# Kernel optimization log

Measured on AMD Instinct MI355X. Metric: run time of the kernel, lower is better.

## Reference

```python
import jax, jax.numpy as jnp
import numpy as np

NUM_HEADS = 32
NUM_KV_HEADS = 8  # num_heads // 4 (GQA)
HEAD_DIM = 64     # hidden_size // num_heads
ROPE_BASE = 10000.0


def _rotate_half(x):
    x1, x2 = jnp.split(x, 2, axis=-1)
    return jnp.concatenate((-x2, x1), axis=-1)


def _rope_cos_sin(seq_len, dtype):
    inv_freq = 1.0 / (ROPE_BASE ** (jnp.arange(0, HEAD_DIM, 2, dtype=jnp.float32) / HEAD_DIM))
    t = jnp.arange(seq_len, dtype=jnp.float32)
    freqs = jnp.outer(t, inv_freq)                 # [S, HEAD_DIM//2]
    emb = jnp.concatenate((freqs, freqs), axis=-1) # [S, HEAD_DIM]
    return jnp.cos(emb).astype(dtype), jnp.sin(emb).astype(dtype)


def setup_inputs() -> dict:
    key = jax.random.key(0)
    ks = jax.random.split(key, 5)
    B, S, H = 1, 2048, 2048
    KV = NUM_KV_HEADS * HEAD_DIM  # 512
    s = 0.02
    return {
        "hidden_states": jax.random.normal(ks[0], (B, S, H), jnp.float32),
        "Wq": jax.random.normal(ks[1], (H, H), jnp.float32) * s,
        "Wk": jax.random.normal(ks[2], (KV, H), jnp.float32) * s,
        "Wv": jax.random.normal(ks[3], (KV, H), jnp.float32) * s,
        "Wo": jax.random.normal(ks[4], (H, H), jnp.float32) * s,
    }


def reference(hidden_states, Wq, Wk, Wv, Wo):
    B, S, H = hidden_states.shape
    dtype = hidden_states.dtype
    # QKV projections (nn.Linear with weight [out,in], no bias)
    q = jnp.einsum("bsh,oh->bso", hidden_states, Wq)
    k = jnp.einsum("bsh,oh->bso", hidden_states, Wk)
    v = jnp.einsum("bsh,oh->bso", hidden_states, Wv)
    q = q.reshape(B, S, NUM_HEADS, HEAD_DIM).transpose(0, 2, 1, 3)      # [B,H,S,D]
    k = k.reshape(B, S, NUM_KV_HEADS, HEAD_DIM).transpose(0, 2, 1, 3)   # [B,KV,S,D]
    v = v.reshape(B, S, NUM_KV_HEADS, HEAD_DIM).transpose(0, 2, 1, 3)
    # RoPE
    cos, sin = _rope_cos_sin(S, dtype)  # [S,D] broadcast over batch/heads
    q = q * cos + _rotate_half(q) * sin
    k = k * cos + _rotate_half(k) * sin
    # GQA: repeat_interleave KV heads
    groups = NUM_HEADS // NUM_KV_HEADS
    k = jnp.repeat(k, groups, axis=1)
    v = jnp.repeat(v, groups, axis=1)
    # Attention: scores in fp32 softmax, causal mask (additive)
    scale = 1.0 / np.sqrt(HEAD_DIM)
    scores = jnp.einsum("bhqd,bhkd->bhqk", q, k) * scale
    causal = jnp.tril(jnp.ones((S, S), dtype=bool))
    scores = jnp.where(causal, scores, jnp.finfo(jnp.float32).min)
    probs = jax.nn.softmax(scores.astype(jnp.float32), axis=-1).astype(dtype)
    attn = jnp.einsum("bhqk,bhkd->bhqd", probs, v)
    attn = attn.transpose(0, 2, 1, 3).reshape(B, S, H)
    return jnp.einsum("bsh,oh->bso", attn, Wo)
```

## Files before the change

### kernel.cpp

```cpp
#include <hip/hip_runtime.h>
#include <hip/hip_bf16.h>
#include <math.h>

typedef __hip_bfloat16 bf16;
typedef __attribute__((ext_vector_type(8))) short short8;
typedef __attribute__((ext_vector_type(4))) short short4v;
typedef __attribute__((ext_vector_type(4))) float floatx4;

#define MFMA16(a, b, c) __builtin_amdgcn_mfma_f32_16x16x32_bf16((a), (b), (c), 0, 0, 0)

typedef const __attribute__((address_space(1))) void* as1_cvp;
typedef __attribute__((address_space(3))) void* as3_vp;

__device__ __forceinline__ void gload_lds16(const bf16* g, bf16* lds_uni) {
    __builtin_amdgcn_global_load_lds((as1_cvp)g, (as3_vp)lds_uni, 16, 0, 0);
}

__global__ __launch_bounds__(256) void cvt_all(
    const float* __restrict__ a0, const float* __restrict__ a1,
    const float* __restrict__ a2, const float* __restrict__ a3,
    const float* __restrict__ a4,
    bf16* __restrict__ d0, bf16* __restrict__ d1, bf16* __restrict__ d2,
    bf16* __restrict__ d3, bf16* __restrict__ d4)
{
    const int b = blockIdx.x;
    const float* src; bf16* dst; int off;
    if (b < 2048)      { src = a0; dst = d0; off = b; }
    else if (b < 4096) { src = a1; dst = d1; off = b - 2048; }
    else if (b < 4608) { src = a2; dst = d2; off = b - 4096; }
    else if (b < 5120) { src = a3; dst = d3; off = b - 4608; }
    else               { src = a4; dst = d4; off = b - 5120; }
    const int i = (off * 256 + threadIdx.x) * 8;
    const float4 x = *(const float4*)(src + i);
    const float4 y = *(const float4*)(src + i + 4);
    bf16 t[8];
    t[0] = __float2bfloat16(x.x); t[1] = __float2bfloat16(x.y);
    t[2] = __float2bfloat16(x.z); t[3] = __float2bfloat16(x.w);
    t[4] = __float2bfloat16(y.x); t[5] = __float2bfloat16(y.y);
    t[6] = __float2bfloat16(y.z); t[7] = __float2bfloat16(y.w);
    *(short8*)(dst + i) = *(const short8*)t;
}

#define GEMM_STAGE6(k0, sA, sB)                                                 \
    gload_lds16(gA + (k0),            (sA));                                    \
    gload_lds16(gA + A64 + (k0),      (sA) + 2048);                             \
    gload_lds16(gB + (k0),            (sB));                                    \
    gload_lds16(gA + (k0) + 32,       (sA) + 4096);                             \
    gload_lds16(gA + A64 + (k0) + 32, (sA) + 6144);                             \
    gload_lds16(gB + (k0) + 32,       (sB) + 2048);

#define GEMM_K_LOOP_DB(KB)                                                      \
    {                                                                           \
        bf16* sA0 = &As[0][0] + w * 512; bf16* sB0 = &Bs[0][0] + w * 512;       \
        bf16* sA1 = &As[1][0] + w * 512; bf16* sB1 = &Bs[1][0] + w * 512;       \
        GEMM_STAGE6(0, sA0, sB0)                                                \
        for (int k0 = 0; k0 < (KB); k0 += 64) {                                 \
            const int cur = (k0 >> 6) & 1;                                      \
            if (k0 + 64 < (KB)) {                                               \
                if (cur == 0) { GEMM_STAGE6(k0 + 64, sA1, sB1) }                \
                else          { GEMM_STAGE6(k0 + 64, sA0, sB0) }                \
                asm volatile("s_waitcnt vmcnt(6)" ::: "memory");                \
            } else {                                                            \
                asm volatile("s_waitcnt vmcnt(0)" ::: "memory");                \
            }                                                                   \
            __builtin_amdgcn_s_barrier();                                       \
            const bf16* Acur = &As[cur][0];                                     \
            const bf16* Bcur = &Bs[cur][0];                                     \
            _Pragma("unroll")                                                   \
            for (int hh = 0; hh < 2; ++hh) {                                    \
                short8 af[2], bfr[4];                                           \
                _Pragma("unroll")                                               \
                for (int i = 0; i < 2; ++i)                                     \
                    af[i] = *(const short8*)&Acur[hh * 4096 + (w * 32 + i * 16 + l15) * 32 + quad * 8]; \
                _Pragma("unroll")                                               \
                for (int j = 0; j < 4; ++j)                                     \
                    bfr[j] = *(const short8*)&Bcur[hh * 2048 + (j * 16 + l15) * 32 + quad * 8]; \
                _Pragma("unroll")                                               \
                for (int i = 0; i < 2; ++i)                                     \
                    _Pragma("unroll")                                           \
                    for (int j = 0; j < 4; ++j)                                 \
                        acc[i][j] = MFMA16(af[i], bfr[j], acc[i][j]);           \
            }                                                                   \
            __builtin_amdgcn_s_barrier();                                       \
        }                                                                       \
    }

__global__ __launch_bounds__(256) void gemm_qkv(
    const bf16* __restrict__ A, const bf16* __restrict__ Wq,
    const bf16* __restrict__ Wk, const bf16* __restrict__ Wv,
    bf16* __restrict__ qb, bf16* __restrict__ kb, bf16* __restrict__ vt)
{
    constexpr int LDK = 2048;
    __shared__ bf16 As[2][128 * 64];
    __shared__ bf16 Bs[2][64 * 64];

    const int tid  = threadIdx.x;
    const int lane = tid & 63;
    const int w    = tid >> 6;
    const int quad = lane >> 4, l15 = lane & 15;
    const int bx = blockIdx.x, by = blockIdx.y;

    const bf16* Bp; int bxl, mode;
    if (bx < 32)      { Bp = Wq; bxl = bx;      mode = 0; }
    else if (bx < 40) { Bp = Wk; bxl = bx - 32; mode = 1; }
    else              { Bp = Wv; bxl = bx - 40; mode = 2; }

    floatx4 acc[2][4];
#pragma unroll
    for (int i = 0; i < 2; ++i)
#pragma unroll
        for (int j = 0; j < 4; ++j) {
            floatx4 z = {0.f, 0.f, 0.f, 0.f};
            acc[i][j] = z;
        }

    const int srow = tid >> 2;
    const int sch  = (tid & 3) * 8;
    const bf16* gA = A  + (size_t)(by * 128 + srow) * LDK + sch;
    const bf16* gB = Bp + (size_t)(bxl * 64 + srow) * LDK + sch;
    const size_t A64 = (size_t)64 * LDK;

    GEMM_K_LOOP_DB(LDK)

    if (mode == 2) {
#pragma unroll
        for (int i = 0; i < 2; ++i)
#pragma unroll
            for (int j = 0; j < 4; ++j) {
                const int col = bxl * 64 + j * 16 + l15;
                const int rowb = by * 128 + w * 32 + i * 16 + quad * 4;
                bf16 t[4];
#pragma unroll
                for (int r = 0; r < 4; ++r) t[r] = __float2bfloat16(acc[i][j][r]);
                *(short4v*)&vt[(size_t)col * 2048 + rowb] = *(const short4v*)t;
            }
    } else {
        bf16* C = (mode == 0) ? qb : kb;
        const int Nn = (mode == 0) ? 2048 : 512;
        const float scale = (mode == 0) ? 0.125f : 1.0f;
        const float LOG2_1E4 = 13.28771237954945f;
        const float ifr0 = exp2f(-((float)l15) * (LOG2_1E4 / 32.f));
        const float ifr1 = exp2f(-((float)(16 + l15)) * (LOG2_1E4 / 32.f));
#pragma unroll
        for (int i = 0; i < 2; ++i) {
#pragma unroll
            for (int r = 0; r < 4; ++r) {
                const int row = by * 128 + w * 32 + i * 16 + quad * 4 + r;
                float s0, c0, s1, c1;
                sincosf((float)row * ifr0, &s0, &c0);
                sincosf((float)row * ifr1, &s1, &c1);
#pragma unroll
                for (int j = 0; j < 4; ++j) {
                    const float x  = acc[i][j][r];
                    const float xp = acc[i][j ^ 2][r];
                    const float cs = (j & 1) ? c1 : c0;
                    const float sn = (j & 1) ? s1 : s0;
                    const float oo = (x * cs + ((j < 2) ? -xp : xp) * sn) * scale;
                    const int col = bxl * 64 + j * 16 + l15;
                    C[(size_t)row * Nn + col] = __float2bfloat16(oo);
                }
            }
        }
    }
}

__global__ __launch_bounds__(256) void gemm_out(
    const bf16* __restrict__ A, const bf16* __restrict__ B, float* __restrict__ C)
{
    constexpr int LDK = 2048;
    __shared__ bf16 As[2][128 * 64];
    __shared__ bf16 Bs[2][64 * 64];

    const int tid  = threadIdx.x;
    const int lane = tid & 63;
    const int w    = tid >> 6;
    const int quad = lane >> 4, l15 = lane & 15;
    const int bx = blockIdx.x, by = blockIdx.y;

    floatx4 acc[2][4];
#pragma unroll
    for (int i = 0; i < 2; ++i)
#pragma unroll
        for (int j = 0; j < 4; ++j) {
            floatx4 z = {0.f, 0.f, 0.f, 0.f};
            acc[i][j] = z;
        }

    const int srow = tid >> 2;
    const int sch  = (tid & 3) * 8;
    const bf16* gA = A + (size_t)(by * 128 + srow) * LDK + sch;
    const bf16* gB = B + (size_t)(bx * 64 + srow) * LDK + sch;
    const size_t A64 = (size_t)64 * LDK;

    GEMM_K_LOOP_DB(LDK)

#pragma unroll
    for (int i = 0; i < 2; ++i)
#pragma unroll
        for (int j = 0; j < 4; ++j)
#pragma unroll
            for (int r = 0; r < 4; ++r) {
                const int row = by * 128 + w * 32 + i * 16 + quad * 4 + r;
                const int col = bx * 64 + j * 16 + l15;
                C[(size_t)row * 2048 + col] = acc[i][j][r];
            }
}

__global__ __launch_bounds__(256) void fattn9(
    const bf16* __restrict__ q, const bf16* __restrict__ k,
    const bf16* __restrict__ vt, bf16* __restrict__ o)
{
    __shared__ bf16 Ks[2][64 * 68];
    __shared__ bf16 Vs[2][64 * 68];
    __shared__ bf16 Ps[4][16 * 68];

    const int tpair = blockIdx.x;
    const int h = blockIdx.y;
    const int kvh = h >> 2;
    const int tid = threadIdx.x, lane = tid & 63, w = tid >> 6;
    const int quad = lane >> 4, l15 = lane & 15;
    bf16* P = Ps[w];

    short ob[8];
#pragma unroll
    for (int e = 0; e < 8; ++e) ob[e] = (short)0x3F80;
    const short8 ones = *(const short8*)ob;

    const int srow = tid >> 3;
    const int ch8  = (tid & 7) * 8;
    const bf16* kg = k  + (size_t)kvh * 64 + ch8;
    const bf16* vg = vt + (size_t)(kvh * 64 + srow) * 2048 + ch8;

#pragma unroll 1
    for (int ph = 0; ph < 2; ++ph) {
        const int a = ph ? (31 - tpair) : tpair;
        const int qrow0 = a * 64 + w * 16;

        short8 qf[2];
#pragma unroll
        for (int ks = 0; ks < 2; ++ks)
            qf[ks] = *(const short8*)&q[(size_t)(qrow0 + l15) * 2048 + h * 64 + ks * 32 + quad * 8];

        floatx4 o_acc[4], l_acc;
#pragma unroll
        for (int n4 = 0; n4 < 4; ++n4) {
            floatx4 z = {0.f, 0.f, 0.f, 0.f};
            o_acc[n4] = z;
        }
        { floatx4 z = {0.f, 0.f, 0.f, 0.f}; l_acc = z; }

        {
            short8 k0 = *(const short8*)(kg + (size_t)srow * 512);
            short8 k1 = *(const short8*)(kg + (size_t)(srow + 32) * 512);
            short8 v0 = *(const short8*)(vg);
            short8 v1 = *(const short8*)(vg + (size_t)32 * 2048);
            *(short8*)&Ks[0][srow * 68 + ch8]        = k0;
            *(short8*)&Ks[0][(srow + 32) * 68 + ch8] = k1;
            *(short8*)&Vs[0][srow * 68 + ch8]        = v0;
            *(short8*)&Vs[0][(srow + 32) * 68 + ch8] = v1;
        }
        __syncthreads();

        for (int kt = 0; kt <= a; ++kt) {
            const int buf = kt & 1;

            short8 nk0, nk1, nv0, nv1;
            if (kt < a) {
                const size_t kr = (size_t)((kt + 1) * 64) * 512;
                nk0 = *(const short8*)(kg + kr + (size_t)srow * 512);
                nk1 = *(const short8*)(kg + kr + (size_t)(srow + 32) * 512);
                nv0 = *(const short8*)(vg + (kt + 1) * 64);
                nv1 = *(const short8*)(vg + (size_t)32 * 2048 + (kt + 1) * 64);
            }

            floatx4 s_acc[4];
#pragma unroll
            for (int n = 0; n < 4; ++n) {
                floatx4 z = {0.f, 0.f, 0.f, 0.f};
                s_acc[n] = z;
            }
#pragma unroll
            for (int n = 0; n < 4; ++n)
#pragma unroll
                for (int ks = 0; ks < 2; ++ks) {
                    const short8 kf = *(const short8*)&Ks[buf][(n * 16 + l15) * 68 + ks * 32 + quad * 8];
                    s_acc[n] = MFMA16(kf, qf[ks], s_acc[n]);
                }

            if (kt < a) {
#pragma unroll
                for (int n = 0; n < 4; ++n) {
                    bf16 t4[4];
#pragma unroll
                    for (int r = 0; r < 4; ++r)
                        t4[r] = __float2bfloat16(__expf(s_acc[n][r]));
                    *(short4v*)&P[l15 * 68 + n * 16 + quad * 4] = *(const short4v*)t4;
                }
            } else {
#pragma unroll
                for (int n = 0; n < 4; ++n) {
                    bf16 t4[4];
#pragma unroll
                    for (int r = 0; r < 4; ++r) {
                        const bool okc = (n * 16 + quad * 4 + r) <= (w * 16 + l15);
                        t4[r] = __float2bfloat16(okc ? __expf(s_acc[n][r]) : 0.f);
                    }
                    *(short4v*)&P[l15 * 68 + n * 16 + quad * 4] = *(const short4v*)t4;
                }
            }

#pragma unroll
            for (int ks2 = 0; ks2 < 2; ++ks2) {
                const short8 pf = *(const short8*)&P[l15 * 68 + ks2 * 32 + quad * 8];
                l_acc = MFMA16(pf, ones, l_acc);
#pragma unroll
                for (int n4 = 0; n4 < 4; ++n4) {
                    const short8 vf = *(const short8*)&Vs[buf][(n4 * 16 + l15) * 68 + ks2 * 32 + quad * 8];
                    o_acc[n4] = MFMA16(pf, vf, o_acc[n4]);
                }
            }

            if (kt < a) {
                *(short8*)&Ks[buf ^ 1][srow * 68 + ch8]        = nk0;
                *(short8*)&Ks[buf ^ 1][(srow + 32) * 68 + ch8] = nk1;
                *(short8*)&Vs[buf ^ 1][srow * 68 + ch8]        = nv0;
                *(short8*)&Vs[buf ^ 1][(srow + 32) * 68 + ch8] = nv1;
            }
            __syncthreads();
        }

#pragma unroll
        for (int n4 = 0; n4 < 4; ++n4)
#pragma unroll
            for (int r = 0; r < 4; ++r) {
                const float val = o_acc[n4][r] / l_acc[r];
                const int row = qrow0 + quad * 4 + r;
                const int col = h * 64 + n4 * 16 + l15;
                o[(size_t)row * 2048 + col] = __float2bfloat16(val);
            }
    }
}

extern "C" void kernel_launch(void* const* d_in, const int* in_sizes, int n_in,
                              void* d_out, int out_size, void* d_ws, size_t ws_size,
                              hipStream_t stream)
{
    const float* hs = (const float*)d_in[0];
    const float* Wq = (const float*)d_in[1];
    const float* Wk = (const float*)d_in[2];
    const float* Wv = (const float*)d_in[3];
    const float* Wo = (const float*)d_in[4];
    float* out = (float*)d_out;

    bf16* ws  = (bf16*)d_ws;
    bf16* hsb = ws;
    bf16* Wqb = ws + 4194304;
    bf16* Wkb = ws + 8388608;
    bf16* Wvb = ws + 9437184;
    bf16* Wob = ws + 10485760;
    bf16* qb  = ws + 14680064;
    bf16* kb  = ws + 18874368;
    bf16* vtb = ws + 19922944;
    bf16* ab  = ws + 20971520;

    dim3 blk(256);
    cvt_all<<<7168, blk, 0, stream>>>(hs, Wq, Wk, Wv, Wo, hsb, Wqb, Wkb, Wvb, Wob);
    gemm_qkv<<<dim3(48, 16), blk, 0, stream>>>(hsb, Wqb, Wkb, Wvb, qb, kb, vtb);
    fattn9<<<dim3(16, 32), blk, 0, stream>>>(qb, kb, vtb, ab);
    gemm_out<<<dim3(32, 16), blk, 0, stream>>>(ab, Wob, out);
}
```

Before: 219.6 us.

## Split attention into 32-row query tiles with 128-thread blocks

The flash-attention kernel now gives each block a 32-row query tile with two waves instead of a 64-row tile with four, and doubles the grid to 32x32 blocks. Each block still pairs a short and a long causal tile to balance work, and the causal mask now compares absolute query and key positions. The aim is more blocks to fill the CUs and finer causal granularity. The cost is that each block loads a full 64-row K/V tile for only 32 query rows, which doubles K/V traffic per query.

```diff
diff --git a/kernel.cpp b/kernel.cpp
--- a/kernel.cpp
+++ b/kernel.cpp
@@ -206,15 +206,15 @@
             }
 }
 
-__global__ __launch_bounds__(256) void fattn9(
+__global__ __launch_bounds__(128) void fattn10(
     const bf16* __restrict__ q, const bf16* __restrict__ k,
     const bf16* __restrict__ vt, bf16* __restrict__ o)
 {
     __shared__ bf16 Ks[2][64 * 68];
     __shared__ bf16 Vs[2][64 * 68];
-    __shared__ bf16 Ps[4][16 * 68];
-
-    const int tpair = blockIdx.x;
+    __shared__ bf16 Ps[2][16 * 68];
+
+    const int tp = blockIdx.x;
     const int h = blockIdx.y;
     const int kvh = h >> 2;
     const int tid = threadIdx.x, lane = tid & 63, w = tid >> 6;
@@ -233,8 +233,9 @@
 
 #pragma unroll 1
     for (int ph = 0; ph < 2; ++ph) {
-        const int a = ph ? (31 - tpair) : tpair;
-        const int qrow0 = a * 64 + w * 16;
+        const int a = ph ? (63 - tp) : tp;
+        const int nkt = (a >> 1) + 1;
+        const int qrow0 = a * 32 + w * 16;
 
         short8 qf[2];
 #pragma unroll
@@ -250,27 +251,26 @@
         { floatx4 z = {0.f, 0.f, 0.f, 0.f}; l_acc = z; }
 
         {
-            short8 k0 = *(const short8*)(kg + (size_t)srow * 512);
-            short8 k1 = *(const short8*)(kg + (size_t)(srow + 32) * 512);
-            short8 v0 = *(const short8*)(vg);
-            short8 v1 = *(const short8*)(vg + (size_t)32 * 2048);
-            *(short8*)&Ks[0][srow * 68 + ch8]        = k0;
-            *(short8*)&Ks[0][(srow + 32) * 68 + ch8] = k1;
-            *(short8*)&Vs[0][srow * 68 + ch8]        = v0;
-            *(short8*)&Vs[0][(srow + 32) * 68 + ch8] = v1;
+#pragma unroll
+            for (int jj = 0; jj < 4; ++jj) {
+                short8 kv_ = *(const short8*)(kg + (size_t)(srow + 16 * jj) * 512);
+                short8 vv_ = *(const short8*)(vg + (size_t)(16 * jj) * 2048);
+                *(short8*)&Ks[0][(srow + 16 * jj) * 68 + ch8] = kv_;
+                *(short8*)&Vs[0][(srow + 16 * jj) * 68 + ch8] = vv_;
+            }
         }
         __syncthreads();
 
-        for (int kt = 0; kt <= a; ++kt) {
+        for (int kt = 0; kt < nkt; ++kt) {
             const int buf = kt & 1;
 
-            short8 nk0, nk1, nv0, nv1;
-            if (kt < a) {
-                const size_t kr = (size_t)((kt + 1) * 64) * 512;
-                nk0 = *(const short8*)(kg + kr + (size_t)srow * 512);
-                nk1 = *(const short8*)(kg + kr + (size_t)(srow + 32) * 512);
-                nv0 = *(const short8*)(vg + (kt + 1) * 64);
-                nv1 = *(const short8*)(vg + (size_t)32 * 2048 + (kt + 1) * 64);
+            short8 nk[4], nv[4];
+            if (kt + 1 < nkt) {
+#pragma unroll
+                for (int jj = 0; jj < 4; ++jj) {
+                    nk[jj] = *(const short8*)(kg + (size_t)((kt + 1) * 64 + srow + 16 * jj) * 512);
+                    nv[jj] = *(const short8*)(vg + (size_t)(16 * jj) * 2048 + (kt + 1) * 64);
+                }
             }
 
             floatx4 s_acc[4];
@@ -287,7 +287,7 @@
                     s_acc[n] = MFMA16(kf, qf[ks], s_acc[n]);
                 }
 
-            if (kt < a) {
+            if (kt + 1 < nkt) {
 #pragma unroll
                 for (int n = 0; n < 4; ++n) {
                     bf16 t4[4];
@@ -297,13 +297,14 @@
                     *(short4v*)&P[l15 * 68 + n * 16 + quad * 4] = *(const short4v*)t4;
                 }
             } else {
+                const int qg = qrow0 + l15;
 #pragma unroll
                 for (int n = 0; n < 4; ++n) {
                     bf16 t4[4];
 #pragma unroll
                     for (int r = 0; r < 4; ++r) {
-                        const bool okc = (n * 16 + quad * 4 + r) <= (w * 16 + l15);
-                        t4[r] = __float2bfloat16(okc ? __expf(s_acc[n][r]) : 0.f);
+                        const int sg = kt * 64 + n * 16 + quad * 4 + r;
+                        t4[r] = __float2bfloat16((sg <= qg) ? __expf(s_acc[n][r]) : 0.f);
                     }
                     *(short4v*)&P[l15 * 68 + n * 16 + quad * 4] = *(const short4v*)t4;
                 }
@@ -320,11 +321,12 @@
                 }
             }
 
-            if (kt < a) {
-                *(short8*)&Ks[buf ^ 1][srow * 68 + ch8]        = nk0;
-                *(short8*)&Ks[buf ^ 1][(srow + 32) * 68 + ch8] = nk1;
-                *(short8*)&Vs[buf ^ 1][srow * 68 + ch8]        = nv0;
-                *(short8*)&Vs[buf ^ 1][(srow + 32) * 68 + ch8] = nv1;
+            if (kt + 1 < nkt) {
+#pragma unroll
+                for (int jj = 0; jj < 4; ++jj) {
+                    *(short8*)&Ks[buf ^ 1][(srow + 16 * jj) * 68 + ch8] = nk[jj];
+                    *(short8*)&Vs[buf ^ 1][(srow + 16 * jj) * 68 + ch8] = nv[jj];
+                }
             }
             __syncthreads();
         }
@@ -366,6 +368,6 @@
     dim3 blk(256);
     cvt_all<<<7168, blk, 0, stream>>>(hs, Wq, Wk, Wv, Wo, hsb, Wqb, Wkb, Wvb, Wob);
     gemm_qkv<<<dim3(48, 16), blk, 0, stream>>>(hsb, Wqb, Wkb, Wvb, qb, kb, vtb);
-    fattn9<<<dim3(16, 32), blk, 0, stream>>>(qb, kb, vtb, ab);
+    fattn10<<<dim3(32, 32), dim3(128), 0, stream>>>(qb, kb, vtb, ab);
     gemm_out<<<dim3(32, 16), blk, 0, stream>>>(ab, Wob, out);
 }
```

New measurement: 225.8 us. 1.03x slower.

## Enlarge GEMM tiles to 128x128 with 2x2 wave layout and BK 32

Applied to the files above, without the earlier changes.

Both projection GEMMs switch from 128x64 output tiles with a K-step of 64 to 128x128 tiles with a K-step of 32. Each wave now computes a 64x64 sub-tile, and grids are halved accordingly. The aim is more operand reuse per LDS load and fewer global bytes per FLOP. The cost is fewer blocks, which leaves gemm_out at one block per CU, plus twice as many barriers per K.

```diff
diff --git a/kernel.cpp b/kernel.cpp
--- a/kernel.cpp
+++ b/kernel.cpp
@@ -41,73 +41,69 @@
     *(short8*)(dst + i) = *(const short8*)t;
 }
 
-#define GEMM_STAGE6(k0, sA, sB)                                                 \
-    gload_lds16(gA + (k0),            (sA));                                    \
-    gload_lds16(gA + A64 + (k0),      (sA) + 2048);                             \
-    gload_lds16(gB + (k0),            (sB));                                    \
-    gload_lds16(gA + (k0) + 32,       (sA) + 4096);                             \
-    gload_lds16(gA + A64 + (k0) + 32, (sA) + 6144);                             \
-    gload_lds16(gB + (k0) + 32,       (sB) + 2048);
-
-#define GEMM_K_LOOP_DB(KB)                                                      \
+#define GEMM_STAGE4(k0, sA, sB)                                                 \
+    gload_lds16(gA + (k0),       (sA));                                         \
+    gload_lds16(gA + K64 + (k0), (sA) + 2048);                                  \
+    gload_lds16(gB + (k0),       (sB));                                         \
+    gload_lds16(gB + K64 + (k0), (sB) + 2048);
+
+#define GEMM_K_LOOP_DB128(KB)                                                   \
     {                                                                           \
         bf16* sA0 = &As[0][0] + w * 512; bf16* sB0 = &Bs[0][0] + w * 512;       \
         bf16* sA1 = &As[1][0] + w * 512; bf16* sB1 = &Bs[1][0] + w * 512;       \
-        GEMM_STAGE6(0, sA0, sB0)                                                \
-        for (int k0 = 0; k0 < (KB); k0 += 64) {                                 \
-            const int cur = (k0 >> 6) & 1;                                      \
-            if (k0 + 64 < (KB)) {                                               \
-                if (cur == 0) { GEMM_STAGE6(k0 + 64, sA1, sB1) }                \
-                else          { GEMM_STAGE6(k0 + 64, sA0, sB0) }                \
-                asm volatile("s_waitcnt vmcnt(6)" ::: "memory");                \
+        GEMM_STAGE4(0, sA0, sB0)                                                \
+        for (int k0 = 0; k0 < (KB); k0 += 32) {                                 \
+            const int cur = (k0 >> 5) & 1;                                      \
+            if (k0 + 32 < (KB)) {                                               \
+                if (cur == 0) { GEMM_STAGE4(k0 + 32, sA1, sB1) }                \
+                else          { GEMM_STAGE4(k0 + 32, sA0, sB0) }                \
+                asm volatile("s_waitcnt vmcnt(4)" ::: "memory");                \
             } else {                                                            \
                 asm volatile("s_waitcnt vmcnt(0)" ::: "memory");                \
             }                                                                   \
             __builtin_amdgcn_s_barrier();                                       \
             const bf16* Acur = &As[cur][0];                                     \
             const bf16* Bcur = &Bs[cur][0];                                     \
+            short8 af[4], bfr[4];                                               \
             _Pragma("unroll")                                                   \
-            for (int hh = 0; hh < 2; ++hh) {                                    \
-                short8 af[2], bfr[4];                                           \
-                _Pragma("unroll")                                               \
-                for (int i = 0; i < 2; ++i)                                     \
-                    af[i] = *(const short8*)&Acur[hh * 4096 + (w * 32 + i * 16 + l15) * 32 + quad * 8]; \
+            for (int i = 0; i < 4; ++i)                                         \
+                af[i] = *(const short8*)&Acur[(wr * 64 + i * 16 + l15) * 32 + quad * 8]; \
+            _Pragma("unroll")                                                   \
+            for (int j = 0; j < 4; ++j)                                         \
+                bfr[j] = *(const short8*)&Bcur[(wc * 64 + j * 16 + l15) * 32 + quad * 8]; \
+            _Pragma("unroll")                                                   \
+            for (int i = 0; i < 4; ++i)                                         \
                 _Pragma("unroll")                                               \
                 for (int j = 0; j < 4; ++j)                                     \
-                    bfr[j] = *(const short8*)&Bcur[hh * 2048 + (j * 16 + l15) * 32 + quad * 8]; \
-                _Pragma("unroll")                                               \
-                for (int i = 0; i < 2; ++i)                                     \
-                    _Pragma("unroll")                                           \
-                    for (int j = 0; j < 4; ++j)                                 \
-                        acc[i][j] = MFMA16(af[i], bfr[j], acc[i][j]);           \
-            }                                                                   \
+                    acc[i][j] = MFMA16(af[i], bfr[j], acc[i][j]);               \
             __builtin_amdgcn_s_barrier();                                       \
         }                                                                       \
     }
 
-__global__ __launch_bounds__(256) void gemm_qkv(
+__global__ __launch_bounds__(256, 4) void gemm_qkv(
     const bf16* __restrict__ A, const bf16* __restrict__ Wq,
     const bf16* __restrict__ Wk, const bf16* __restrict__ Wv,
     bf16* __restrict__ qb, bf16* __restrict__ kb, bf16* __restrict__ vt)
 {
     constexpr int LDK = 2048;
-    __shared__ bf16 As[2][128 * 64];
-    __shared__ bf16 Bs[2][64 * 64];
+    __shared__ bf16 As[2][128 * 32];
+    __shared__ bf16 Bs[2][128 * 32];
 
     const int tid  = threadIdx.x;
     const int lane = tid & 63;
     const int w    = tid >> 6;
+    const int wr   = w >> 1, wc = w & 1;
     const int quad = lane >> 4, l15 = lane & 15;
     const int bx = blockIdx.x, by = blockIdx.y;
 
     const bf16* Bp; int bxl, mode;
-    if (bx < 32)      { Bp = Wq; bxl = bx;      mode = 0; }
-    else if (bx < 40) { Bp = Wk; bxl = bx - 32; mode = 1; }
-    else              { Bp = Wv; bxl = bx - 40; mode = 2; }
-
-    floatx4 acc[2][4];
-#pragma unroll
-    for (int i = 0; i < 2; ++i)
+    if (bx < 16)      { Bp = Wq; bxl = bx;      mode = 0; }
+    else if (bx < 20) { Bp = Wk; bxl = bx - 16; mode = 1; }
+    else              { Bp = Wv; bxl = bx - 20; mode = 2; }
+
+    floatx4 acc[4][4];
+#pragma unroll
+    for (int i = 0; i < 4; ++i)
 #pragma unroll
         for (int j = 0; j < 4; ++j) {
             floatx4 z = {0.f, 0.f, 0.f, 0.f};
@@ -117,18 +113,18 @@
     const int srow = tid >> 2;
     const int sch  = (tid & 3) * 8;
     const bf16* gA = A  + (size_t)(by * 128 + srow) * LDK + sch;
-    const bf16* gB = Bp + (size_t)(bxl * 64 + srow) * LDK + sch;
-    const size_t A64 = (size_t)64 * LDK;
-
-    GEMM_K_LOOP_DB(LDK)
+    const bf16* gB = Bp + (size_t)(bxl * 128 + srow) * LDK + sch;
+    const size_t K64 = (size_t)64 * LDK;
+
+    GEMM_K_LOOP_DB128(LDK)
 
     if (mode == 2) {
 #pragma unroll
-        for (int i = 0; i < 2; ++i)
+        for (int i = 0; i < 4; ++i)
 #pragma unroll
             for (int j = 0; j < 4; ++j) {
-                const int col = bxl * 64 + j * 16 + l15;
-                const int rowb = by * 128 + w * 32 + i * 16 + quad * 4;
+                const int col = bxl * 128 + wc * 64 + j * 16 + l15;
+                const int rowb = by * 128 + wr * 64 + i * 16 + quad * 4;
                 bf16 t[4];
 #pragma unroll
                 for (int r = 0; r < 4; ++r) t[r] = __float2bfloat16(acc[i][j][r]);
@@ -142,10 +138,10 @@
         const float ifr0 = exp2f(-((float)l15) * (LOG2_1E4 / 32.f));
         const float ifr1 = exp2f(-((float)(16 + l15)) * (LOG2_1E4 / 32.f));
 #pragma unroll
-        for (int i = 0; i < 2; ++i) {
+        for (int i = 0; i < 4; ++i) {
 #pragma unroll
             for (int r = 0; r < 4; ++r) {
-                const int row = by * 128 + w * 32 + i * 16 + quad * 4 + r;
+                const int row = by * 128 + wr * 64 + i * 16 + quad * 4 + r;
                 float s0, c0, s1, c1;
                 sincosf((float)row * ifr0, &s0, &c0);
                 sincosf((float)row * ifr1, &s1, &c1);
@@ -156,7 +152,7 @@
                     const float cs = (j & 1) ? c1 : c0;
                     const float sn = (j & 1) ? s1 : s0;
                     const float oo = (x * cs + ((j < 2) ? -xp : xp) * sn) * scale;
-                    const int col = bxl * 64 + j * 16 + l15;
+                    const int col = bxl * 128 + wc * 64 + j * 16 + l15;
                     C[(size_t)row * Nn + col] = __float2bfloat16(oo);
                 }
             }
@@ -164,22 +160,23 @@
     }
 }
 
-__global__ __launch_bounds__(256) void gemm_out(
+__global__ __launch_bounds__(256, 4) void gemm_out(
     const bf16* __restrict__ A, const bf16* __restrict__ B, float* __restrict__ C)
 {
     constexpr int LDK = 2048;
-    __shared__ bf16 As[2][128 * 64];
-    __shared__ bf16 Bs[2][64 * 64];
+    __shared__ bf16 As[2][128 * 32];
+    __shared__ bf16 Bs[2][128 * 32];
 
     const int tid  = threadIdx.x;
     const int lane = tid & 63;
     const int w    = tid >> 6;
+    const int wr   = w >> 1, wc = w & 1;
     const int quad = lane >> 4, l15 = lane & 15;
     const int bx = blockIdx.x, by = blockIdx.y;
 
-    floatx4 acc[2][4];
-#pragma unroll
-    for (int i = 0; i < 2; ++i)
+    floatx4 acc[4][4];
+#pragma unroll
+    for (int i = 0; i < 4; ++i)
 #pragma unroll
         for (int j = 0; j < 4; ++j) {
             floatx4 z = {0.f, 0.f, 0.f, 0.f};
@@ -189,19 +186,19 @@
     const int srow = tid >> 2;
     const int sch  = (tid & 3) * 8;
     const bf16* gA = A + (size_t)(by * 128 + srow) * LDK + sch;
-    const bf16* gB = B + (size_t)(bx * 64 + srow) * LDK + sch;
-    const size_t A64 = (size_t)64 * LDK;
-
-    GEMM_K_LOOP_DB(LDK)
-
-#pragma unroll
-    for (int i = 0; i < 2; ++i)
+    const bf16* gB = B + (size_t)(bx * 128 + srow) * LDK + sch;
+    const size_t K64 = (size_t)64 * LDK;
+
+    GEMM_K_LOOP_DB128(LDK)
+
+#pragma unroll
+    for (int i = 0; i < 4; ++i)
 #pragma unroll
         for (int j = 0; j < 4; ++j)
 #pragma unroll
             for (int r = 0; r < 4; ++r) {
-                const int row = by * 128 + w * 32 + i * 16 + quad * 4 + r;
-                const int col = bx * 64 + j * 16 + l15;
+                const int row = by * 128 + wr * 64 + i * 16 + quad * 4 + r;
+                const int col = bx * 128 + wc * 64 + j * 16 + l15;
                 C[(size_t)row * 2048 + col] = acc[i][j][r];
             }
 }
@@ -365,7 +362,7 @@
 
     dim3 blk(256);
     cvt_all<<<7168, blk, 0, stream>>>(hs, Wq, Wk, Wv, Wo, hsb, Wqb, Wkb, Wvb, Wob);
-    gemm_qkv<<<dim3(48, 16), blk, 0, stream>>>(hsb, Wqb, Wkb, Wvb, qb, kb, vtb);
+    gemm_qkv<<<dim3(24, 16), blk, 0, stream>>>(hsb, Wqb, Wkb, Wvb, qb, kb, vtb);
     fattn9<<<dim3(16, 32), blk, 0, stream>>>(qb, kb, vtb, ab);
-    gemm_out<<<dim3(32, 16), blk, 0, stream>>>(ab, Wob, out);
-}
+    gemm_out<<<dim3(16, 16), blk, 0, stream>>>(ab, Wob, out);
+}
```

After: 235.3 us. +7.1%, slower.
